# Optimization experiments

Hardware: AMD Instinct MI355X
Metric: run time of the kernel (lower is better)

## Reference

```python
import jax, jax.numpy as jnp
import numpy as np

B = 8192
N_NODES = 48        # max_atom_num
ATOM_TYPES = 8
M_DIM = ATOM_TYPES + 1   # 9, one-hot classes
MAX_DIM = N_NODES + ATOM_TYPES  # 56
B_DIM = 3           # bond/relation types
GC1, GC2 = 128, 64  # graph_conv_dim
AUX = 128           # aux_dim
LIN = [128, 64]     # linear_dim


def _linear(key, fan_in, fan_out, bias=True):
    kw, kb = jax.random.split(key)
    lim = 1.0 / np.sqrt(fan_in)
    W = jax.random.uniform(kw, (fan_in, fan_out), minval=-lim, maxval=lim, dtype=jnp.float32)
    if bias:
        b = jax.random.uniform(kb, (fan_out,), minval=-lim, maxval=lim, dtype=jnp.float32)
        return W, b
    return W


def setup_inputs() -> dict:
    key = jax.random.key(0)
    ks = jax.random.split(key, 24)
    N = jax.random.randint(ks[0], (B, MAX_DIM), 0, 9)
    adj = jax.random.uniform(ks[1], (B, B_DIM, N_NODES, N_NODES), dtype=jnp.float32)
    W1, b1 = _linear(ks[2], M_DIM, GC1)
    W2, b2 = _linear(ks[3], GC1, GC2)
    agg_sW, agg_sb = _linear(ks[4], GC2 + M_DIM, AUX)
    agg_tW, agg_tb = _linear(ks[5], GC2 + M_DIM, AUX)
    l1W, l1b = _linear(ks[6], AUX, LIN[0])
    l2W, l2b = _linear(ks[7], LIN[0], LIN[1])
    f1 = _linear(ks[8], LIN[1], 32, bias=False)
    f2 = _linear(ks[9], 32, MAX_DIM, bias=False)
    s1 = _linear(ks[10], LIN[1], 32, bias=False)
    s2 = _linear(ks[11], 32, MAX_DIM, bias=False)
    e1 = _linear(ks[12], LIN[1], 32, bias=False)
    e2 = _linear(ks[13], 32, B_DIM, bias=False)
    t1W, t1b = _linear(ks[14], LIN[1], 32)
    t2W, t2b = _linear(ks[15], 32, 2)
    v1W, v1b = _linear(ks[16], LIN[1], 32)
    v2W, v2b = _linear(ks[17], 32, 16)
    v3W, v3b = _linear(ks[18], 16, 1)
    return dict(N=N, adj=adj, W1=W1, b1=b1, W2=W2, b2=b2,
                agg_sW=agg_sW, agg_sb=agg_sb, agg_tW=agg_tW, agg_tb=agg_tb,
                l1W=l1W, l1b=l1b, l2W=l2W, l2b=l2b,
                f1=f1, f2=f2, s1=s1, s2=s2, e1=e1, e2=e2,
                t1W=t1W, t1b=t1b, t2W=t2W, t2b=t2b,
                v1W=v1W, v1b=v1b, v2W=v2W, v2b=v2b, v3W=v3W, v3b=v3b)


def reference(N, adj, W1, b1, W2, b2, agg_sW, agg_sb, agg_tW, agg_tb,
              l1W, l1b, l2W, l2b, f1, f2, s1, s2, e1, e2,
              t1W, t1b, t2W, t2b, v1W, v1b, v2W, v2b, v3W, v3b):
    lrelu = lambda x: jax.nn.leaky_relu(x, 0.1)
    node = N[:, :N_NODES]
    onehot = jax.nn.one_hot(node, M_DIM, dtype=jnp.float32)  # [B,n,9]

    # --- GraphConvolution: diag-normalized adjacency, two relational layers ---
    # D = diag(1 / (rowsum(adj) + 1)) ; adj_n = D @ adj  (eye adds 1 per row)
    deg = 1.0 / (jnp.sum(adj, axis=3) + 1.0)        # [B,r,n]
    adj_n = adj * deg[..., None]                     # [B,r,n,n]
    h1 = onehot @ W1 + b1                            # [B,n,128] (shared across relations)
    h = jnp.tanh(jnp.einsum('brij,bjd->bid', adj_n, h1) + h1)
    h2 = h @ W2 + b2                                 # [B,n,64]
    h_out = jnp.tanh(jnp.einsum('brij,bjd->bid', adj_n, h2) + h2)

    # --- GraphAggregation: gated sigmoid*tanh pooling over nodes, tanh activation ---
    ann = jnp.concatenate([h_out, onehot], axis=-1)  # [B,n,73]
    gate = jax.nn.sigmoid(ann @ agg_sW + agg_sb) * jnp.tanh(ann @ agg_tW + agg_tb)
    g = jnp.tanh(jnp.sum(gate, axis=1))              # [B,128]

    # --- linear stack (no nonlinearity between, dropout=0) ---
    hfeat = (g @ l1W + l1b) @ l2W + l2b              # [B,64]

    # --- heads ---
    out1 = lrelu(hfeat @ f1) @ f2                    # [B,56]
    out2 = lrelu(hfeat @ s1) @ s2                    # [B,56]
    oute = lrelu(hfeat @ e1) @ e2                    # [B,3]
    outs = lrelu(hfeat @ t1W + t1b) @ t2W + t2b      # [B,2]
    value = lrelu(lrelu(hfeat @ v1W + v1b) @ v2W + v2b) @ v3W + v3b  # [B,1]

    # --- masked softmaxes (Mask_first: existing atoms; Mask_second: existing+new atom slots minus first) ---
    idx = jnp.arange(MAX_DIM)
    exists = (N > 0) & (idx[None, :] < N_NODES)      # [B,56]
    mask_first = exists.astype(out1.dtype)
    p1 = jax.nn.softmax((mask_first - 1.0) * 10000.0 + out1, axis=1)
    first = jnp.argmax(p1, axis=1)                   # deterministic stand-in for Categorical sample
    mask_second = (exists | (idx[None, :] >= N_NODES)).astype(out2.dtype)
    mask_second = jnp.where(idx[None, :] == first[:, None], 0.0, mask_second)
    p2 = jax.nn.softmax((mask_second - 1.0) * 10000.0 + out2, axis=1)
    pe = jax.nn.softmax(oute, axis=1)
    pt = jax.nn.softmax(outs, axis=1)
    # concat all deterministic outputs: [B, 56+56+3+2+1]
    return jnp.concatenate([p1, p2, pe, pt, value], axis=-1)
```

## Files before the change

kernel.cpp:

```cpp
#include <hip/hip_runtime.h>
#include <math.h>

#define NN 48
#define MD 56

__device__ __forceinline__ float rcp_f(float x){
#if __has_builtin(__builtin_amdgcn_rcpf)
  return __builtin_amdgcn_rcpf(x);
#else
  return 1.0f/x;
#endif
}

__global__ __launch_bounds__(256, 4)
void policy_fwd(const int* __restrict__ Nmat, const float* __restrict__ adj,
                const float* __restrict__ W1, const float* __restrict__ b1,
                const float* __restrict__ W2, const float* __restrict__ b2,
                const float* __restrict__ agg_sW, const float* __restrict__ agg_sb,
                const float* __restrict__ agg_tW, const float* __restrict__ agg_tb,
                const float* __restrict__ l1W, const float* __restrict__ l1b,
                const float* __restrict__ l2W, const float* __restrict__ l2b,
                const float* __restrict__ f1, const float* __restrict__ f2,
                const float* __restrict__ s1, const float* __restrict__ s2,
                const float* __restrict__ e1, const float* __restrict__ e2,
                const float* __restrict__ t1W, const float* __restrict__ t1b,
                const float* __restrict__ t2W, const float* __restrict__ t2b,
                const float* __restrict__ v1W, const float* __restrict__ v1b,
                const float* __restrict__ v2W, const float* __restrict__ v2b,
                const float* __restrict__ v3W, const float* __restrict__ v3b,
                float* __restrict__ out)
{
  __shared__ __align__(16) float sA[NN*48];
  __shared__ __align__(16) float sHB[3264];
  __shared__ __align__(16) float sH2[3264];
  __shared__ __align__(16) float sEP[1280];
  __shared__ int   sNi[MD];

  const int b   = blockIdx.x;
  const int tid = threadIdx.x;
  const float* adjB = adj + (size_t)b * (3*NN*NN);
  float* sDeg = &sHB[3104];

  if (tid < MD) sNi[tid] = Nmat[b*MD + tid];

  {
    const int lane = tid & 15, grp = tid >> 4;
    for (int p = 0; p < 9; ++p) {
      const int row = p*16 + grp;
      const float* rp = adjB + row*NN;
      float s = rp[lane] + rp[lane+16] + rp[lane+32];
      s += __shfl_down(s, 8, 16);
      s += __shfl_down(s, 4, 16);
      s += __shfl_down(s, 2, 16);
      s += __shfl_down(s, 1, 16);
      if (lane == 0) sDeg[row] = 1.0f/(s + 1.0f);
    }
  }
  for (int o = tid; o < 1152; o += 256) sEP[o] = W1[o] + b1[o & 127];
  __syncthreads();

  for (int o = tid; o < NN*NN; o += 256) {
    const int i = o / NN, j = o - i*NN;
    const float v = adjB[i*NN + j]          * sDeg[i]
                  + adjB[(NN + i)*NN + j]   * sDeg[NN + i]
                  + adjB[(2*NN + i)*NN + j] * sDeg[2*NN + i];
    sA[i*48 + j] = v;
  }
  __syncthreads();

  const int i2 = (tid >> 4)*3, d2 = (tid & 15)*4;

  float acc2[3][4] = {};
  #pragma unroll
  for (int r = 0; r < 2; ++r) {
    const int dg = r*64 + d2;
    {
      float acc[3][4] = {};
      #pragma unroll 4
      for (int k = 0; k < NN; ++k) {
        const int nk = sNi[k];
        const float4 bv = *(const float4*)&sEP[nk*128 + dg];
        const float* ap = &sA[i2*48 + k];
        #pragma unroll
        for (int ii = 0; ii < 3; ++ii) {
          const float a = ap[ii*48];
          acc[ii][0] = fmaf(a, bv.x, acc[ii][0]);
          acc[ii][1] = fmaf(a, bv.y, acc[ii][1]);
          acc[ii][2] = fmaf(a, bv.z, acc[ii][2]);
          acc[ii][3] = fmaf(a, bv.w, acc[ii][3]);
        }
      }
      #pragma unroll
      for (int ii = 0; ii < 3; ++ii) {
        const float4 rv = *(const float4*)&sEP[sNi[i2+ii]*128 + dg];
        float4 o;
        o.x = tanhf(acc[ii][0] + rv.x);
        o.y = tanhf(acc[ii][1] + rv.y);
        o.z = tanhf(acc[ii][2] + rv.z);
        o.w = tanhf(acc[ii][3] + rv.w);
        *(float4*)&sHB[(i2+ii)*68 + d2] = o;
      }
    }
    __syncthreads();
    {
      const float* W2r = W2 + (size_t)r*64*64;
      #pragma unroll 8
      for (int k = 0; k < 64; ++k) {
        const float4 bv = *(const float4*)&W2r[k*64 + d2];
        const float* ap = &sHB[i2*68 + k];
        #pragma unroll
        for (int ii = 0; ii < 3; ++ii) {
          const float a = ap[ii*68];
          acc2[ii][0] = fmaf(a, bv.x, acc2[ii][0]);
          acc2[ii][1] = fmaf(a, bv.y, acc2[ii][1]);
          acc2[ii][2] = fmaf(a, bv.z, acc2[ii][2]);
          acc2[ii][3] = fmaf(a, bv.w, acc2[ii][3]);
        }
      }
    }
    __syncthreads();
  }
  {
    const float4 bb = *(const float4*)&b2[d2];
    #pragma unroll
    for (int ii = 0; ii < 3; ++ii) {
      float4 o;
      o.x = acc2[ii][0] + bb.x; o.y = acc2[ii][1] + bb.y;
      o.z = acc2[ii][2] + bb.z; o.w = acc2[ii][3] + bb.w;
      *(float4*)&sH2[(i2+ii)*68 + d2] = o;
    }
  }
  __syncthreads();

  {
    float acc[3][4] = {};
    #pragma unroll 4
    for (int k = 0; k < NN; ++k) {
      const float4 bv = *(const float4*)&sH2[k*68 + d2];
      const float* ap = &sA[i2*48 + k];
      #pragma unroll
      for (int ii = 0; ii < 3; ++ii) {
        const float a = ap[ii*48];
        acc[ii][0] = fmaf(a, bv.x, acc[ii][0]);
        acc[ii][1] = fmaf(a, bv.y, acc[ii][1]);
        acc[ii][2] = fmaf(a, bv.z, acc[ii][2]);
        acc[ii][3] = fmaf(a, bv.w, acc[ii][3]);
      }
    }
    #pragma unroll
    for (int ii = 0; ii < 3; ++ii) {
      const float4 rv = *(const float4*)&sH2[(i2+ii)*68 + d2];
      float4 o;
      o.x = tanhf(acc[ii][0] + rv.x);
      o.y = tanhf(acc[ii][1] + rv.y);
      o.z = tanhf(acc[ii][2] + rv.z);
      o.w = tanhf(acc[ii][3] + rv.w);
      *(float4*)&sHB[(i2+ii)*68 + d2] = o;
    }
  }
  __syncthreads();

  {
    float as0[3][4] = {}, as1[3][4] = {}, at0[3][4] = {}, at1[3][4] = {};
    #pragma unroll 4
    for (int k = 0; k < 64; ++k) {
      const float4 bs0 = *(const float4*)&agg_sW[k*128 + d2];
      const float4 bs1 = *(const float4*)&agg_sW[k*128 + 64 + d2];
      const float4 bt0 = *(const float4*)&agg_tW[k*128 + d2];
      const float4 bt1 = *(const float4*)&agg_tW[k*128 + 64 + d2];
      const float* ap = &sHB[i2*68 + k];
      #pragma unroll
      for (int ii = 0; ii < 3; ++ii) {
        const float a = ap[ii*68];
        as0[ii][0] = fmaf(a, bs0.x, as0[ii][0]);
        as0[ii][1] = fmaf(a, bs0.y, as0[ii][1]);
        as0[ii][2] = fmaf(a, bs0.z, as0[ii][2]);
        as0[ii][3] = fmaf(a, bs0.w, as0[ii][3]);
        as1[ii][0] = fmaf(a, bs1.x, as1[ii][0]);
        as1[ii][1] = fmaf(a, bs1.y, as1[ii][1]);
        as1[ii][2] = fmaf(a, bs1.z, as1[ii][2]);
        as1[ii][3] = fmaf(a, bs1.w, as1[ii][3]);
        at0[ii][0] = fmaf(a, bt0.x, at0[ii][0]);
        at0[ii][1] = fmaf(a, bt0.y, at0[ii][1]);
        at0[ii][2] = fmaf(a, bt0.z, at0[ii][2]);
        at0[ii][3] = fmaf(a, bt0.w, at0[ii][3]);
        at1[ii][0] = fmaf(a, bt1.x, at1[ii][0]);
        at1[ii][1] = fmaf(a, bt1.y, at1[ii][1]);
        at1[ii][2] = fmaf(a, bt1.z, at1[ii][2]);
        at1[ii][3] = fmaf(a, bt1.w, at1[ii][3]);
      }
    }
    float p0[4] = {0.f,0.f,0.f,0.f}, p1[4] = {0.f,0.f,0.f,0.f};
    const float4 bsb0 = *(const float4*)&agg_sb[d2];
    const float4 bsb1 = *(const float4*)&agg_sb[64 + d2];
    const float4 btb0 = *(const float4*)&agg_tb[d2];
    const float4 btb1 = *(const float4*)&agg_tb[64 + d2];
    const float bsb0a[4] = {bsb0.x,bsb0.y,bsb0.z,bsb0.w};
    const float bsb1a[4] = {bsb1.x,bsb1.y,bsb1.z,bsb1.w};
    const float btb0a[4] = {btb0.x,btb0.y,btb0.z,btb0.w};
    const float btb1a[4] = {btb1.x,btb1.y,btb1.z,btb1.w};
    #pragma unroll
    for (int ii = 0; ii < 3; ++ii) {
      const int t = sNi[i2+ii];
      const float* gs = &agg_sW[(64 + t)*128];
      const float* gt = &agg_tW[(64 + t)*128];
      #pragma unroll
      for (int dd = 0; dd < 4; ++dd) {
        const float sg0 = 1.0f/(1.0f + expf(-(as0[ii][dd] + gs[d2+dd]      + bsb0a[dd])));
        const float tg0 = tanhf(at0[ii][dd] + gt[d2+dd]      + btb0a[dd]);
        p0[dd] = fmaf(sg0, tg0, p0[dd]);
        const float sg1 = 1.0f/(1.0f + expf(-(as1[ii][dd] + gs[64+d2+dd] + bsb1a[dd])));
        const float tg1 = tanhf(at1[ii][dd] + gt[64+d2+dd] + btb1a[dd]);
        p1[dd] = fmaf(sg1, tg1, p1[dd]);
      }
    }
    const int grp = tid >> 4;
    *(float4*)&sEP[grp*64 + d2] = *(float4*)p0;
    *(float4*)&sH2[grp*64 + d2] = *(float4*)p1;
  }
  __syncthreads();
  if (tid < 64) {
    float s = 0.0f;
    #pragma unroll
    for (int g = 0; g < 16; ++g) s += sEP[g*64 + tid];
    sEP[1024 + tid] = s;
  } else if (tid < 128) {
    const int m = tid - 64;
    float s = 0.0f;
    #pragma unroll
    for (int g = 0; g < 16; ++g) s += sH2[g*64 + m];
    sEP[1024 + 64 + m] = s;
  }
  __syncthreads();

  float* sT = sHB;
  const float* sGsum = &sEP[1024];
  if (tid < 128) sT[tid + 1024] = tanhf(sGsum[tid]);
  __syncthreads();
  if (tid < 128) {
    float a = l1b[tid];
    for (int k = 0; k < 128; ++k) a = fmaf(sT[1024+k], l1W[k*128 + tid], a);
    sT[1152 + tid] = a;
  }
  __syncthreads();
  if (tid < 64) {
    float a = l2b[tid];
    for (int k = 0; k < 128; ++k) a = fmaf(sT[1152+k], l2W[k*64 + tid], a);
    sT[1280 + tid] = a;
  }
  __syncthreads();
  if (tid < 160) {
    const int hh = tid >> 5, j = tid & 31;
    const float* Wp = (hh==0) ? f1 : (hh==1) ? s1 : (hh==2) ? e1 : (hh==3) ? t1W : v1W;
    float a = (hh==3) ? t1b[j] : (hh==4) ? v1b[j] : 0.0f;
    for (int k = 0; k < 64; ++k) a = fmaf(sT[1280+k], Wp[k*32 + j], a);
    sT[1344 + tid] = (a > 0.0f) ? a : 0.1f*a;
  }
  __syncthreads();
  if (tid < 56) {
    float a = 0.0f;
    for (int k = 0; k < 32; ++k) a = fmaf(sT[1344+k], f2[k*56 + tid], a);
    sT[1504 + tid] = a;
  } else if (tid < 112) {
    const int m = tid - 56; float a = 0.0f;
    for (int k = 0; k < 32; ++k) a = fmaf(sT[1376+k], s2[k*56 + m], a);
    sT[1560 + m] = a;
  } else if (tid < 115) {
    const int m = tid - 112; float a = 0.0f;
    for (int k = 0; k < 32; ++k) a = fmaf(sT[1408+k], e2[k*3 + m], a);
    sT[1616 + m] = a;
  } else if (tid < 117) {
    const int m = tid - 115; float a = t2b[m];
    for (int k = 0; k < 32; ++k) a = fmaf(sT[1440+k], t2W[k*2 + m], a);
    sT[1619 + m] = a;
  } else if (tid < 133) {
    const int m = tid - 117; float a = v2b[m];
    for (int k = 0; k < 32; ++k) a = fmaf(sT[1472+k], v2W[k*16 + m], a);
    sT[1624 + m] = (a > 0.0f) ? a : 0.1f*a;
  }
  __syncthreads();
  if (tid == 0) {
    float a = v3b[0];
    for (int k = 0; k < 16; ++k) a = fmaf(sT[1624+k], v3W[k], a);
    sT[1640] = a;
  }
  __syncthreads();

  if (tid < 64) {
    const int m = tid;
    const bool inb = (m < MD);
    const bool ex  = inb && (sNi[m] > 0) && (m < NN);
    const size_t ob = (size_t)b * 118;

    float lg1 = inb ? (sT[1504+m] + (ex ? 0.0f : -10000.0f)) : -INFINITY;
    float mv = lg1; int mi = inb ? m : 1000;
    #pragma unroll
    for (int off = 32; off > 0; off >>= 1) {
      const float ov = __shfl_down(mv, off);
      const int   oi = __shfl_down(mi, off);
      if (ov > mv || (ov == mv && oi < mi)) { mv = ov; mi = oi; }
    }
    mv = __shfl(mv, 0);
    const int first = __shfl(mi, 0);
    float ev = inb ? __expf(lg1 - mv) : 0.0f;
    float sum1 = ev;
    #pragma unroll
    for (int off = 32; off > 0; off >>= 1) sum1 += __shfl_down(sum1, off);
    sum1 = rcp_f(__shfl(sum1, 0));
    if (inb) out[ob + m] = ev * sum1;

    const bool m2 = inb && ((ex || m >= NN) && (m != first));
    float lg2 = inb ? (sT[1560+m] + (m2 ? 0.0f : -10000.0f)) : -INFINITY;
    float mv2 = lg2;
    #pragma unroll
    for (int off = 32; off > 0; off >>= 1) mv2 = fmaxf(mv2, __shfl_down(mv2, off));
    mv2 = __shfl(mv2, 0);
    float ev2 = inb ? __expf(lg2 - mv2) : 0.0f;
    float sum2 = ev2;
    #pragma unroll
    for (int off = 32; off > 0; off >>= 1) sum2 += __shfl_down(sum2, off);
    sum2 = rcp_f(__shfl(sum2, 0));
    if (inb) out[ob + 56 + m] = ev2 * sum2;

    if (m < 3) {
      const float x0 = sT[1616], x1 = sT[1617], x2 = sT[1618];
      const float mx = fmaxf(x0, fmaxf(x1, x2));
      const float q0 = __expf(x0-mx), q1 = __expf(x1-mx), q2 = __expf(x2-mx);
      out[ob + 112 + m] = ((m==0) ? q0 : (m==1) ? q1 : q2) / (q0+q1+q2);
    }
    if (m < 2) {
      const float x0 = sT[1619], x1 = sT[1620];
      const float mx = fmaxf(x0, x1);
      const float q0 = __expf(x0-mx), q1 = __expf(x1-mx);
      out[ob + 115 + m] = ((m==0) ? q0 : q1) / (q0+q1);
    }
    if (m == 0) out[ob + 117] = sT[1640];
  }
}

extern "C" void kernel_launch(void* const* d_in, const int* in_sizes, int n_in,
                              void* d_out, int out_size, void* d_ws, size_t ws_size,
                              hipStream_t stream) {
  (void)n_in; (void)out_size; (void)d_ws; (void)ws_size;
  const int B = in_sizes[0] / MD;
  policy_fwd<<<dim3(B), dim3(256), 0, stream>>>(
      (const int*)d_in[0],  (const float*)d_in[1],
      (const float*)d_in[2],  (const float*)d_in[3],
      (const float*)d_in[4],  (const float*)d_in[5],
      (const float*)d_in[6],  (const float*)d_in[7],
      (const float*)d_in[8],  (const float*)d_in[9],
      (const float*)d_in[10], (const float*)d_in[11],
      (const float*)d_in[12], (const float*)d_in[13],
      (const float*)d_in[14], (const float*)d_in[15],
      (const float*)d_in[16], (const float*)d_in[17],
      (const float*)d_in[18], (const float*)d_in[19],
      (const float*)d_in[20], (const float*)d_in[21],
      (const float*)d_in[22], (const float*)d_in[23],
      (const float*)d_in[24], (const float*)d_in[25],
      (const float*)d_in[26], (const float*)d_in[27],
      (const float*)d_in[28], (const float*)d_in[29],
      (float*)d_out);
}
```

Measured before the change: 946.7 us.

## Shrink shared memory by aliasing H buffers and raise occupancy to six blocks

Drops the separate sH2 buffer and keeps the hidden layers in sHB with a new padded row layout (64 floats plus 4 pad every 4 rows). The residual reads are moved into registers before an added barrier so the second graph-conv layer can overwrite in place, and the gating partials reuse sA. The node types are pre-scaled by 128 to save index multiplies. The goal is to cut LDS use per block so six 256-thread blocks fit per CU instead of four, at the cost of an extra barrier and a tighter register budget.

```diff
diff --git a/kernel.cpp b/kernel.cpp
--- a/kernel.cpp
+++ b/kernel.cpp
@@ -12,7 +12,9 @@
 #endif
 }
 
-__global__ __launch_bounds__(256, 4)
+#define HROW(r) ((r)*64 + (((r)>>2)<<2))
+
+__global__ __launch_bounds__(256, 6)
 void policy_fwd(const int* __restrict__ Nmat, const float* __restrict__ adj,
                 const float* __restrict__ W1, const float* __restrict__ b1,
                 const float* __restrict__ W2, const float* __restrict__ b2,
@@ -30,18 +32,17 @@
                 const float* __restrict__ v3W, const float* __restrict__ v3b,
                 float* __restrict__ out)
 {
-  __shared__ __align__(16) float sA[NN*48];
-  __shared__ __align__(16) float sHB[3264];
-  __shared__ __align__(16) float sH2[3264];
-  __shared__ __align__(16) float sEP[1280];
+  __shared__ __align__(16) float sA[2304];
+  __shared__ __align__(16) float sHB[3120];
+  __shared__ __align__(16) float sEP[1152];
   __shared__ int   sNi[MD];
 
   const int b   = blockIdx.x;
   const int tid = threadIdx.x;
   const float* adjB = adj + (size_t)b * (3*NN*NN);
-  float* sDeg = &sHB[3104];
-
-  if (tid < MD) sNi[tid] = Nmat[b*MD + tid];
+  float* sDeg = sHB;
+
+  if (tid < MD) sNi[tid] = Nmat[b*MD + tid] * 128;
 
   {
     const int lane = tid & 15, grp = tid >> 4;
@@ -69,6 +70,7 @@
   __syncthreads();
 
   const int i2 = (tid >> 4)*3, d2 = (tid & 15)*4;
+  float* hr[3] = { &sHB[HROW(i2)], &sHB[HROW(i2+1)], &sHB[HROW(i2+2)] };
 
   float acc2[3][4] = {};
   #pragma unroll
@@ -79,7 +81,7 @@
       #pragma unroll 4
       for (int k = 0; k < NN; ++k) {
         const int nk = sNi[k];
-        const float4 bv = *(const float4*)&sEP[nk*128 + dg];
+        const float4 bv = *(const float4*)&sEP[nk + dg];
         const float* ap = &sA[i2*48 + k];
         #pragma unroll
         for (int ii = 0; ii < 3; ++ii) {
@@ -92,13 +94,13 @@
       }
       #pragma unroll
       for (int ii = 0; ii < 3; ++ii) {
-        const float4 rv = *(const float4*)&sEP[sNi[i2+ii]*128 + dg];
+        const float4 rv = *(const float4*)&sEP[sNi[i2+ii] + dg];
         float4 o;
         o.x = tanhf(acc[ii][0] + rv.x);
         o.y = tanhf(acc[ii][1] + rv.y);
         o.z = tanhf(acc[ii][2] + rv.z);
         o.w = tanhf(acc[ii][3] + rv.w);
-        *(float4*)&sHB[(i2+ii)*68 + d2] = o;
+        *(float4*)&hr[ii][d2] = o;
       }
     }
     __syncthreads();
@@ -107,10 +109,9 @@
       #pragma unroll 8
       for (int k = 0; k < 64; ++k) {
         const float4 bv = *(const float4*)&W2r[k*64 + d2];
-        const float* ap = &sHB[i2*68 + k];
         #pragma unroll
         for (int ii = 0; ii < 3; ++ii) {
-          const float a = ap[ii*68];
+          const float a = hr[ii][k];
           acc2[ii][0] = fmaf(a, bv.x, acc2[ii][0]);
           acc2[ii][1] = fmaf(a, bv.y, acc2[ii][1]);
           acc2[ii][2] = fmaf(a, bv.z, acc2[ii][2]);
@@ -127,7 +128,7 @@
       float4 o;
       o.x = acc2[ii][0] + bb.x; o.y = acc2[ii][1] + bb.y;
       o.z = acc2[ii][2] + bb.z; o.w = acc2[ii][3] + bb.w;
-      *(float4*)&sH2[(i2+ii)*68 + d2] = o;
+      *(float4*)&hr[ii][d2] = o;
     }
   }
   __syncthreads();
@@ -136,7 +137,7 @@
     float acc[3][4] = {};
     #pragma unroll 4
     for (int k = 0; k < NN; ++k) {
-      const float4 bv = *(const float4*)&sH2[k*68 + d2];
+      const float4 bv = *(const float4*)&sHB[HROW(k) + d2];
       const float* ap = &sA[i2*48 + k];
       #pragma unroll
       for (int ii = 0; ii < 3; ++ii) {
@@ -147,15 +148,18 @@
         acc[ii][3] = fmaf(a, bv.w, acc[ii][3]);
       }
     }
+    float4 rv[3];
+    #pragma unroll
+    for (int ii = 0; ii < 3; ++ii) rv[ii] = *(const float4*)&hr[ii][d2];
+    __syncthreads();
     #pragma unroll
     for (int ii = 0; ii < 3; ++ii) {
-      const float4 rv = *(const float4*)&sH2[(i2+ii)*68 + d2];
       float4 o;
-      o.x = tanhf(acc[ii][0] + rv.x);
-      o.y = tanhf(acc[ii][1] + rv.y);
-      o.z = tanhf(acc[ii][2] + rv.z);
-      o.w = tanhf(acc[ii][3] + rv.w);
-      *(float4*)&sHB[(i2+ii)*68 + d2] = o;
+      o.x = tanhf(acc[ii][0] + rv[ii].x);
+      o.y = tanhf(acc[ii][1] + rv[ii].y);
+      o.z = tanhf(acc[ii][2] + rv[ii].z);
+      o.w = tanhf(acc[ii][3] + rv[ii].w);
+      *(float4*)&hr[ii][d2] = o;
     }
   }
   __syncthreads();
@@ -168,10 +172,9 @@
       const float4 bs1 = *(const float4*)&agg_sW[k*128 + 64 + d2];
       const float4 bt0 = *(const float4*)&agg_tW[k*128 + d2];
       const float4 bt1 = *(const float4*)&agg_tW[k*128 + 64 + d2];
-      const float* ap = &sHB[i2*68 + k];
       #pragma unroll
       for (int ii = 0; ii < 3; ++ii) {
-        const float a = ap[ii*68];
+        const float a = hr[ii][k];
         as0[ii][0] = fmaf(a, bs0.x, as0[ii][0]);
         as0[ii][1] = fmaf(a, bs0.y, as0[ii][1]);
         as0[ii][2] = fmaf(a, bs0.z, as0[ii][2]);
@@ -202,12 +205,12 @@
     #pragma unroll
     for (int ii = 0; ii < 3; ++ii) {
       const int t = sNi[i2+ii];
-      const float* gs = &agg_sW[(64 + t)*128];
-      const float* gt = &agg_tW[(64 + t)*128];
+      const float* gs = agg_sW + 64*128 + t;
+      const float* gt = agg_tW + 64*128 + t;
       #pragma unroll
       for (int dd = 0; dd < 4; ++dd) {
-        const float sg0 = 1.0f/(1.0f + expf(-(as0[ii][dd] + gs[d2+dd]      + bsb0a[dd])));
-        const float tg0 = tanhf(at0[ii][dd] + gt[d2+dd]      + btb0a[dd]);
+        const float sg0 = 1.0f/(1.0f + expf(-(as0[ii][dd] + gs[d2+dd]    + bsb0a[dd])));
+        const float tg0 = tanhf(at0[ii][dd] + gt[d2+dd]    + btb0a[dd]);
         p0[dd] = fmaf(sg0, tg0, p0[dd]);
         const float sg1 = 1.0f/(1.0f + expf(-(as1[ii][dd] + gs[64+d2+dd] + bsb1a[dd])));
         const float tg1 = tanhf(at1[ii][dd] + gt[64+d2+dd] + btb1a[dd]);
@@ -216,7 +219,7 @@
     }
     const int grp = tid >> 4;
     *(float4*)&sEP[grp*64 + d2] = *(float4*)p0;
-    *(float4*)&sH2[grp*64 + d2] = *(float4*)p1;
+    *(float4*)&sA [grp*64 + d2] = *(float4*)p1;
   }
   __syncthreads();
   if (tid < 64) {
@@ -228,7 +231,7 @@
     const int m = tid - 64;
     float s = 0.0f;
     #pragma unroll
-    for (int g = 0; g < 16; ++g) s += sH2[g*64 + m];
+    for (int g = 0; g < 16; ++g) s += sA[g*64 + m];
     sEP[1024 + 64 + m] = s;
   }
   __syncthreads();
```

After: 1.305 ms. 37.9% more time.
